# Optimization experiments

Hardware: AMD Instinct MI355X
Metric: run time of the kernel (lower is better)

The kernel has to match this reference:

```python
import jax, jax.numpy as jnp
import numpy as np

B, T = 1024, 39
NUM_C, NUM_STU, NUM_E, EMB = 123, 100000, 50000, 256
H = 123
IN1 = NUM_C + EMB  # 379


def setup_inputs() -> dict:
    key = jax.random.key(0)
    ks = jax.random.split(key, 32)
    f = lambda k, shp, s: jax.random.normal(k, shp, dtype=jnp.float32) * s
    inp = {}
    inp["q_maritx"] = jax.random.uniform(ks[0], (B, T, NUM_C), dtype=jnp.float32)
    inp["q_maritx_next"] = jax.random.uniform(ks[1], (B, T, NUM_C), dtype=jnp.float32)
    inp["concept"] = jax.random.randint(ks[2], (B, T), 0, NUM_C + 1)
    inp["s_id"] = jax.random.randint(ks[3], (B, 1), 0, NUM_STU + 1)
    inp["e_id"] = jax.random.randint(ks[4], (B, T), 0, NUM_E + 1)
    inp["r"] = jax.random.randint(ks[5], (B, T), 0, 2)
    inp["q_next"] = jax.random.randint(ks[6], (B, T), 0, NUM_E + 1)
    inp["concept_next"] = jax.random.randint(ks[7], (B, T), 0, NUM_C + 1)
    # learned parameters
    inp["emb_problem"] = f(ks[8], (NUM_E + 1, EMB), 1.0)
    inp["student_W"] = f(ks[9], (NUM_STU + 1, NUM_C), 1.0)
    inp["k_diff_W"] = f(ks[10], (NUM_E + 1, NUM_C), 1.0)
    inp["e_disc_W"] = f(ks[11], (NUM_E + 1, 1), 1.0)
    inp["answer_W"] = f(ks[12], (2, EMB), 1.0)
    inp["zz_W"] = f(ks[13], (NUM_C, NUM_C), 0.05)
    inp["zz_b"] = jnp.zeros((NUM_C,), jnp.float32)
    inp["d_t"] = f(ks[14], (1,), 1.0)
    inp["d_e"] = f(ks[15], (1,), 1.0)
    inp["W_ih"] = f(ks[16], (H, IN1), 0.05)
    inp["b_ih"] = jnp.zeros((H,), jnp.float32)
    inp["W_hh"] = f(ks[17], (H, H), 0.05)
    inp["b_hh"] = jnp.zeros((H,), jnp.float32)
    inp["W_tg"] = f(ks[18], (H, 1), 0.05)
    inp["b_tg"] = jnp.zeros((H,), jnp.float32)
    inp["W_z"] = f(ks[19], (H, IN1 + H), 0.05)
    inp["b_z"] = jnp.zeros((H,), jnp.float32)
    inp["W_h"] = f(ks[20], (H, IN1 + H), 0.05)
    inp["b_h"] = jnp.zeros((H,), jnp.float32)
    inp["p1_W"] = f(ks[21], (256, 502), 0.05)
    inp["p1_b"] = jnp.zeros((256,), jnp.float32)
    inp["p2_W"] = f(ks[22], (123, 256), 0.05)
    inp["p2_b"] = jnp.zeros((123,), jnp.float32)
    inp["p3_W"] = f(ks[23], (1, 123), 0.05)
    inp["p3_b"] = jnp.zeros((1,), jnp.float32)
    return inp


def _forward(q_maritx, q_maritx_next, emb_problem, student_W, k_diff_W, e_disc_W,
             answer_W, zz_W, zz_b, d_t, d_e, W_ih, b_ih, W_hh, b_hh, W_tg, b_tg,
             W_z, b_z, W_h, b_h, p1_W, p1_b, p2_W, p2_b, p3_W, p3_b,
             s_id, e_id, r, q_next):
    Bc, Tc = e_id.shape
    e_next_emb = emb_problem[q_next]                       # [B,T,256]
    s_prof = jax.nn.sigmoid(student_W[s_id])               # [B,1,123] (broadcasts vs repeat(1,39,1))
    k_diff = jax.nn.sigmoid(k_diff_W[e_id])                # [B,T,123]
    e_disc = jax.nn.sigmoid(e_disc_W[e_id]) * d_e          # [B,T,1]
    r_emb = answer_W[r]                                    # [B,T,256]
    concept_ab = jnp.einsum('btk,hk->bth', q_maritx, zz_W) + zz_b  # [B,T,123]
    x1 = jnp.concatenate([concept_ab * s_prof, r_emb], axis=-1)    # [B,T,379]
    # --- time-gated RNN: h_t = tanh(W_ih x_t + W_hh h + b) * sigmoid(tg(t)) ---
    Xp = jnp.einsum('bti,hi->bth', x1, W_ih) + b_ih
    tvec = jnp.arange(Tc, dtype=Xp.dtype)[:, None]
    gates = jax.nn.sigmoid(tvec * W_tg[:, 0][None, :] + b_tg)      # [T,123]
    h0 = jnp.zeros((Bc, W_hh.shape[0]), Xp.dtype)

    def step1(h, xs):
        xp, g = xs
        h = jnp.tanh(xp + h @ W_hh.T + b_hh) * g
        return h, h

    _, ys1 = jax.lax.scan(step1, h0, (Xp.transpose(1, 0, 2), gates))
    out_zz = ys1.transpose(1, 0, 2)                        # [B,T,123]
    # --- GRU-like cell (W_r unused in original forward) ---
    input_x1 = e_disc * (d_t * s_prof + (1.0 - d_t) * out_zz - k_diff) * q_maritx
    x2 = jnp.concatenate([input_x1, r_emb], axis=-1)       # [B,T,379]
    nin = x2.shape[-1]
    Wz_x, Wz_h = W_z[:, :nin], W_z[:, nin:]
    Wh_x, Wh_h = W_h[:, :nin], W_h[:, nin:]
    Zx = jnp.einsum('bti,hi->bth', x2, Wz_x) + b_z
    Hx = jnp.einsum('bti,hi->bth', x2, Wh_x) + b_h

    def step2(h, xs):
        zx, hx = xs
        z = jax.nn.sigmoid(zx + h @ Wz_h.T)
        ht = jnp.tanh(hx + h @ Wh_h.T)
        h = (1.0 - z) * h + z * ht
        return h, h

    _, ys2 = jax.lax.scan(step2, h0, (Zx.transpose(1, 0, 2), Hx.transpose(1, 0, 2)))
    outputs = ys2.transpose(1, 0, 2)                       # [B,T,123]
    hcat = jnp.concatenate([outputs, e_next_emb, q_maritx_next], axis=-1)  # [B,T,502]
    o1 = jax.nn.sigmoid(hcat @ p1_W.T + p1_b)  # dropout as identity (deterministic reference)
    o2 = jax.nn.sigmoid(o1 @ p2_W.T + p2_b)
    return jax.nn.sigmoid(o2 @ p3_W.T + p3_b)              # [B,T,1]


def reference(q_maritx, q_maritx_next, emb_problem, student_W, k_diff_W, e_disc_W,
              answer_W, zz_W, zz_b, d_t, d_e, W_ih, b_ih, W_hh, b_hh, W_tg, b_tg,
              W_z, b_z, W_h, b_h, p1_W, p1_b, p2_W, p2_b, p3_W, p3_b,
              concept, s_id, e_id, r, q_next, concept_next):
    # concept / concept_next embeddings are computed but unused in the original output
    return _forward(q_maritx, q_maritx_next, emb_problem, student_W, k_diff_W,
                    e_disc_W, answer_W, zz_W, zz_b, d_t, d_e, W_ih, b_ih, W_hh,
                    b_hh, W_tg, b_tg, W_z, b_z, W_h, b_h, p1_W, p1_b, p2_W,
                    p2_b, p3_W, p3_b, s_id, e_id, r, q_next)
```

## Files before the change

kernel.cpp:

```cpp
#include <hip/hip_runtime.h>
#include <hip/hip_bf16.h>

#define NRB 39936
#define BB 1024
#define TT 39
#define CC 123
#define EMBD 256
#define PCH 136

typedef __attribute__((ext_vector_type(8))) short short8;
typedef __attribute__((ext_vector_type(4))) float floatx4;
typedef unsigned short us;

__device__ __forceinline__ float rcp_(float x){ return __builtin_amdgcn_rcpf(x); }
__device__ __forceinline__ float fsig(float x){ return rcp_(1.f + __expf(-x)); }
__device__ __forceinline__ float ftanh(float x){
  float ax = __builtin_fabsf(x);
  float e = __expf(-2.f*ax);
  float r = (1.f - e) * rcp_(1.f + e);
  return __builtin_copysignf(r, x);
}
__device__ __forceinline__ us f2bf(float x){
  union { float f; unsigned u; } v; v.f = x;
  unsigned r = v.u + 0x7FFFu + ((v.u >> 16) & 1u);
  return (us)(r >> 16);
}
__device__ __forceinline__ float bf2f(us u){
  union { unsigned u; float f; } v; v.u = ((unsigned)u) << 16; return v.f;
}

__device__ __forceinline__ void gl_lds16(void* lds, const void* g){
  __builtin_amdgcn_global_load_lds(
      (const __attribute__((address_space(1))) unsigned int*)g,
      (__attribute__((address_space(3))) unsigned int*)lds, 16, 0, 0);
}

#define G_RC 6
#define G_CW 1088
#define G_CAST 2496
#define G_HCAT 1872
#define G_PRE (G_RC + G_CW + G_CAST + G_HCAT)

__global__ __launch_bounds__(256) void k_pre(
    const float* __restrict__ W_ih, const float* __restrict__ W_z,
    const float* __restrict__ W_h, const float* __restrict__ answer_W,
    const float* __restrict__ zz_W, const float* __restrict__ W_hh,
    const float* __restrict__ p1_W, const float* __restrict__ p2_W,
    const float* __restrict__ emb, const int* __restrict__ q_next,
    const float* __restrict__ qmn, const float* __restrict__ q_m,
    float* __restrict__ rtab, us* __restrict__ wts,
    us* __restrict__ p1bf, us* __restrict__ p2bf,
    us* __restrict__ qbf, us* __restrict__ Abf)
{
  const int blk = blockIdx.x, tid = threadIdx.x;
  if (blk < G_RC){
    int which = blk >> 1, j = blk & 1, h = tid;
    if (h >= CC) return;
    const float* W; int stride;
    if (which==0){ W=W_ih; stride=379; } else if (which==1){ W=W_z; stride=502; } else { W=W_h; stride=502; }
    const float* a = answer_W + j*EMBD;
    const float* w = W + (size_t)h*stride + CC;
    float acc = 0.f;
    #pragma unroll 8
    for (int i=0;i<EMBD;i++) acc += w[i]*a[i];
    rtab[(which*2+j)*128 + h] = acc;
    return;
  }
  if (blk < G_RC + G_CW){
    int i = (blk - G_RC)*256 + tid;
    if (i < 7*16384){
      int w = i >> 14, idx = i & 16383, n = idx >> 7, k = idx & 127;
      float v = 0.f;
      if (n < CC && k < CC){
        if      (w==0) v = zz_W[n*CC + k];
        else if (w==1) v = W_ih[n*379 + k];
        else if (w==2) v = W_z [n*502 + k];
        else if (w==3) v = W_h [n*502 + k];
        else if (w==4) v = W_hh[n*CC + k];
        else if (w==5) v = W_z [n*502 + 379 + k];
        else           v = W_h [n*502 + 379 + k];
      }
      wts[i] = f2bf(v);
      return;
    }
    int j = i - 7*16384;
    if (j < 256*512){
      int n = j >> 9, k = j & 511;
      float v;
      if      (k < 379) v = p1_W[n*502 + k + 123];
      else if (k < 384) v = 0.f;
      else if (k < 507) v = p1_W[n*502 + (k - 384)];
      else              v = 0.f;
      p1bf[j] = f2bf(v);
      return;
    }
    j -= 256*512;
    if (j < 128*256){
      int n = j >> 8, k = j & 255;
      p2bf[j] = f2bf(n < CC ? p2_W[n*256 + k] : 0.f);
    }
    return;
  }
  if (blk < G_RC + G_CW + G_CAST){
    const size_t total = (size_t)NRB*128;
    for (size_t i = (size_t)(blk - G_RC - G_CW)*256 + tid; i < total; i += (size_t)G_CAST*256){
      int col = (int)(i & 127); size_t rp = i >> 7;
      int t = (int)(rp >> 10), b = (int)(rp & 1023);
      float v = (col < CC) ? q_m[((size_t)b*TT + t)*CC + col] : 0.f;
      qbf[i] = f2bf(v);
    }
    return;
  }
  {
    const size_t nchunk = (size_t)NRB*48;
    for (size_t c = (size_t)(blk - G_RC - G_CW - G_CAST)*256 + tid; c < nchunk; c += (size_t)G_HCAT*256){
      size_t row = c / 48;
      int c0 = (int)(c - row*48) * 8;
      short8 o;
      if (c0 < 256){
        int qn = q_next[row];
        float4 v0 = *(const float4*)(emb + (size_t)qn*EMBD + c0);
        float4 v1 = *(const float4*)(emb + (size_t)qn*EMBD + c0 + 4);
        o[0]=f2bf(v0.x); o[1]=f2bf(v0.y); o[2]=f2bf(v0.z); o[3]=f2bf(v0.w);
        o[4]=f2bf(v1.x); o[5]=f2bf(v1.y); o[6]=f2bf(v1.z); o[7]=f2bf(v1.w);
      } else {
        int j0 = c0 - 256;
        #pragma unroll
        for (int jj=0;jj<8;jj++){
          int j = j0 + jj;
          o[jj] = (j < CC) ? f2bf(qmn[row*CC + j]) : (short)0;
        }
      }
      *(short8*)(Abf + row*512 + c0) = o;
    }
  }
}

__global__ __launch_bounds__(256) void k_zz_elem(
    const us* __restrict__ X, const us* __restrict__ W,
    const float* __restrict__ zz_b,
    const float* __restrict__ q_m, const int* __restrict__ s_id,
    const int* __restrict__ e_id, const float* __restrict__ student_W,
    const float* __restrict__ k_diff_W, const float* __restrict__ e_disc_W,
    const float* __restrict__ d_t_p, const float* __restrict__ d_e_p,
    us* __restrict__ x1a, us* __restrict__ pre2, us* __restrict__ cqb)
{
  __shared__ __align__(16) us Asl[16][64][8];
  const int tid = threadIdx.x, w = tid >> 6, l = tid & 63, q = l >> 4, r16 = l & 15;
  const int rTile = blockIdx.x*64;
  short8 bfr[2][4];
  #pragma unroll
  for (int nt=0;nt<2;nt++){
    int n = w*32 + nt*16 + r16;
    #pragma unroll
    for (int kt=0;kt<4;kt++)
      bfr[nt][kt] = *(const short8*)(W + (size_t)n*128 + kt*32 + q*8);
  }
  #pragma unroll
  for (int i=0;i<4;i++){
    int seg = i*4 + w;
    gl_lds16(&Asl[seg][l][0], X + (size_t)(rTile+l)*128 + seg*8);
  }
  floatx4 acc[4][2];
  #pragma unroll
  for (int mt=0;mt<4;mt++){
    #pragma unroll
    for (int nt=0;nt<2;nt++){ acc[mt][nt][0]=0.f; acc[mt][nt][1]=0.f; acc[mt][nt][2]=0.f; acc[mt][nt][3]=0.f; }
  }
  __syncthreads();
  #pragma unroll
  for (int kt=0;kt<4;kt++){
    short8 af[4];
    #pragma unroll
    for (int mt=0;mt<4;mt++) af[mt] = *(const short8*)&Asl[kt*4+q][mt*16+r16][0];
    #pragma unroll
    for (int mt=0;mt<4;mt++){
      #pragma unroll
      for (int nt=0;nt<2;nt++)
        acc[mt][nt] = __builtin_amdgcn_mfma_f32_16x16x32_bf16(af[mt], bfr[nt][kt], acc[mt][nt], 0,0,0);
    }
  }
  const float dt = d_t_p[0], de = d_e_p[0];
  float zzb[2]; int colv[2];
  #pragma unroll
  for (int nt=0;nt<2;nt++){
    int col = w*32 + nt*16 + r16; colv[nt] = col;
    zzb[nt] = (col < CC) ? zz_b[col] : 0.f;
  }
  const int t = rTile >> 10;
  #pragma unroll
  for (int mt=0;mt<4;mt++){
    #pragma unroll
    for (int i=0;i<4;i++){
      int row = rTile + mt*16 + q*4 + i;
      int b = row & 1023;
      int g = b*TT + t;
      int btile = b >> 4, r = b & 15;
      int sid = s_id[b];
      int e   = e_id[g];
      float ed = fsig(e_disc_W[e]) * de;
      size_t base = ((size_t)t*64 + btile)*2048;
      #pragma unroll
      for (int nt=0;nt<2;nt++){
        int col = colv[nt];
        float x1v = 0.f, p2v = 0.f, cqv = 0.f;
        if (col < CC){
          float ab = acc[mt][nt][i] + zzb[nt];
          float sp = fsig(student_W[(size_t)sid*CC + col]);
          float kd = fsig(k_diff_W[(size_t)e*CC + col]);
          float qv = q_m[(size_t)g*CC + col];
          x1v = ab*sp;
          p2v = ed*(dt*sp - kd)*qv;
          cqv = ed*(1.f - dt)*qv;
        }
        x1a[base + (size_t)(((col>>5)*64 + ((col>>3)&3)*16 + r)*8) + (col&7)] = f2bf(x1v);
        size_t off = base + (size_t)(((col>>5)*64 + ((r>>2))*16 + (col&15))*8) + ((col>>4)&1)*4 + (r&3);
        pre2[off] = f2bf(p2v);
        cqb[off]  = f2bf(cqv);
      }
    }
  }
}

__global__ __launch_bounds__(256,1) void k_mid(
    const us* __restrict__ x1a, const us* __restrict__ pre2, const us* __restrict__ cqb,
    const us* __restrict__ Wih, const us* __restrict__ Whh,
    const us* __restrict__ Wzx, const us* __restrict__ Whx,
    const us* __restrict__ Wzh, const us* __restrict__ Whh2,
    const float* __restrict__ b_ih, const float* __restrict__ b_z, const float* __restrict__ b_h,
    const float* __restrict__ W_tg, const float* __restrict__ b_tg,
    const float* __restrict__ rtab, const int* __restrict__ r_idx,
    us* __restrict__ Abf)
{
  __shared__ __align__(16) us x1s[2][2048];
  __shared__ __align__(16) us p2s[2][2048];
  __shared__ __align__(16) us cqs[2][2048];
  __shared__ __align__(16) us h1s[2][16*PCH];
  __shared__ __align__(16) us x2s[16*PCH];
  __shared__ __align__(16) us h2r[4][16*PCH];
  __shared__ int rint[640];
  const int tid = threadIdx.x, w = tid >> 6, l = tid & 63, q = l >> 4, r16 = l & 15;
  const int bbase = blockIdx.x*16;

  short8 fih[2][4], fhh[2][4], fzx[2][4], fhx[2][4], fzh[2][4], fh2[2][4];
  float bih[2], bz[2], bh[2], wgv[2], bgv[2];
  float r1v[2][2], r2v[2][2], r3v[2][2];
  int colv[2];
  #pragma unroll
  for (int nt=0;nt<2;nt++){
    int n = w*32 + nt*16 + r16; colv[nt] = n;
    #pragma unroll
    for (int kt=0;kt<4;kt++){
      fih[nt][kt] = *(const short8*)(Wih  + (size_t)n*128 + kt*32 + q*8);
      fhh[nt][kt] = *(const short8*)(Whh  + (size_t)n*128 + kt*32 + q*8);
      fzx[nt][kt] = *(const short8*)(Wzx  + (size_t)n*128 + kt*32 + q*8);
      fhx[nt][kt] = *(const short8*)(Whx  + (size_t)n*128 + kt*32 + q*8);
      fzh[nt][kt] = *(const short8*)(Wzh  + (size_t)n*128 + kt*32 + q*8);
      fh2[nt][kt] = *(const short8*)(Whh2 + (size_t)n*128 + kt*32 + q*8);
    }
    bool v = n < CC;
    bih[nt] = v ? b_ih[n] : 0.f;
    bz [nt] = v ? b_z [n] : 0.f;
    bh [nt] = v ? b_h [n] : 0.f;
    wgv[nt] = v ? W_tg[n] : 0.f;
    bgv[nt] = v ? b_tg[n] : 0.f;
    r1v[0][nt] = v ? rtab[0*128+n] : 0.f;  r1v[1][nt] = v ? rtab[1*128+n] : 0.f;
    r2v[0][nt] = v ? rtab[2*128+n] : 0.f;  r2v[1][nt] = v ? rtab[3*128+n] : 0.f;
    r3v[0][nt] = v ? rtab[4*128+n] : 0.f;  r3v[1][nt] = v ? rtab[5*128+n] : 0.f;
  }
  for (int i = tid; i < TT*16; i += 256){
    int t = i >> 4, row = i & 15;
    rint[i] = r_idx[(size_t)(bbase+row)*TT + t];
  }
  for (int i = tid; i < 16*PCH; i += 256){ h1s[0][i] = 0; h2r[3][i] = 0; }
  {
    size_t base = (size_t)blockIdx.x*2048;
    gl_lds16(&x1s[0][tid*8], x1a  + base + tid*8);
    gl_lds16(&p2s[0][tid*8], pre2 + base + tid*8);
    gl_lds16(&cqs[0][tid*8], cqb  + base + tid*8);
  }
  floatx4 hold[2];
  #pragma unroll
  for (int nt=0;nt<2;nt++){ hold[nt][0]=0.f; hold[nt][1]=0.f; hold[nt][2]=0.f; hold[nt][3]=0.f; }
  __syncthreads();

  for (int t=0; t<TT; t++){
    const int cur = t & 1, nxt = cur ^ 1, rb1 = t & 1, wb1 = rb1 ^ 1;
    if (t < TT-1){
      size_t base = ((size_t)(t+1)*64 + blockIdx.x)*2048;
      gl_lds16(&x1s[nxt][tid*8], x1a  + base + tid*8);
      gl_lds16(&p2s[nxt][tid*8], pre2 + base + tid*8);
      gl_lds16(&cqs[nxt][tid*8], cqb  + base + tid*8);
    }
    short8 a1[4], ah[4], a2p[4];
    #pragma unroll
    for (int kt=0;kt<4;kt++){
      a1[kt]  = *(const short8*)&x1s[cur][(kt*64 + l)*8];
      ah[kt]  = *(const short8*)&h1s[rb1][r16*PCH + kt*32 + q*8];
      a2p[kt] = *(const short8*)&h2r[(t+3)&3][r16*PCH + kt*32 + q*8];
    }
    short8 pc8 = *(const short8*)&p2s[cur][(w*64 + l)*8];
    short8 cc8 = *(const short8*)&cqs[cur][(w*64 + l)*8];
    int rs[4];
    #pragma unroll
    for (int i=0;i<4;i++) rs[i] = rint[t*16 + q*4 + i];
    floatx4 acc1[2], az[2], ahh[2];
    #pragma unroll
    for (int nt=0;nt<2;nt++){
      #pragma unroll
      for (int i=0;i<4;i++){
        acc1[nt][i] = bih[nt] + (rs[i] ? r1v[1][nt] : r1v[0][nt]);
        az  [nt][i] = bz [nt] + (rs[i] ? r2v[1][nt] : r2v[0][nt]);
        ahh [nt][i] = bh [nt] + (rs[i] ? r3v[1][nt] : r3v[0][nt]);
      }
    }
    #pragma unroll
    for (int kt=0;kt<4;kt++){
      #pragma unroll
      for (int nt=0;nt<2;nt++){
        acc1[nt] = __builtin_amdgcn_mfma_f32_16x16x32_bf16(a1[kt],  fih[nt][kt], acc1[nt], 0,0,0);
        acc1[nt] = __builtin_amdgcn_mfma_f32_16x16x32_bf16(ah[kt],  fhh[nt][kt], acc1[nt], 0,0,0);
        az [nt]  = __builtin_amdgcn_mfma_f32_16x16x32_bf16(a2p[kt], fzh[nt][kt], az [nt], 0,0,0);
        ahh[nt]  = __builtin_amdgcn_mfma_f32_16x16x32_bf16(a2p[kt], fh2[nt][kt], ahh[nt], 0,0,0);
      }
    }
    #pragma unroll
    for (int nt=0;nt<2;nt++){
      float g = fsig((float)t*wgv[nt] + bgv[nt]);
      #pragma unroll
      for (int i=0;i<4;i++){
        float h1 = ftanh(acc1[nt][i]) * g;
        h1s[wb1][(q*4+i)*PCH + colv[nt]] = f2bf(h1);
        float pcv = bf2f((us)pc8[nt*4+i]);
        float ccv = bf2f((us)cc8[nt*4+i]);
        x2s[(q*4+i)*PCH + colv[nt]] = f2bf(pcv + ccv*h1);
      }
    }
    __syncthreads();
    short8 ax2[4];
    #pragma unroll
    for (int kt=0;kt<4;kt++) ax2[kt] = *(const short8*)&x2s[r16*PCH + kt*32 + q*8];
    #pragma unroll
    for (int kt=0;kt<4;kt++){
      #pragma unroll
      for (int nt=0;nt<2;nt++){
        az [nt] = __builtin_amdgcn_mfma_f32_16x16x32_bf16(ax2[kt], fzx[nt][kt], az [nt], 0,0,0);
        ahh[nt] = __builtin_amdgcn_mfma_f32_16x16x32_bf16(ax2[kt], fhx[nt][kt], ahh[nt], 0,0,0);
      }
    }
    #pragma unroll
    for (int nt=0;nt<2;nt++){
      #pragma unroll
      for (int i=0;i<4;i++){
        float z  = fsig(az[nt][i]);
        float th = ftanh(ahh[nt][i]);
        float hv = hold[nt][i] + z*(th - hold[nt][i]);
        hold[nt][i] = hv;
        h2r[t&3][(q*4+i)*PCH + colv[nt]] = f2bf(hv);
      }
    }
    __syncthreads();
    if ((t & 3) == 3 || t == TT-1){
      int ns = (t & 3) + 1;
      int r = tid >> 4, c8 = tid & 15;
      for (int s=0; s<ns; s++){
        int td = t - (t & 3) + s;
        short8 vch = *(const short8*)&h2r[s][r*PCH + c8*8];
        *(short8*)(Abf + ((size_t)(bbase + r)*TT + td)*512 + 384 + c8*8) = vch;
      }
      __syncthreads();
    }
  }
}

__global__ __launch_bounds__(256) void k_o1_mfma(
    const us* __restrict__ Abf, const us* __restrict__ p1bf,
    const float* __restrict__ p1_b, us* __restrict__ o1bf)
{
  __shared__ __align__(16) us Asl[8][64][8];
  __shared__ __align__(16) us Bsl[8][256][8];
  const int tid = threadIdx.x;
  const int w = tid >> 6, l = tid & 63;
  const int q = l >> 4, r16 = l & 15;
  const int rTile = blockIdx.x * 64;
  floatx4 acc[4][4];
  #pragma unroll
  for (int a=0;a<4;a++){
    #pragma unroll
    for (int b=0;b<4;b++){ acc[a][b][0]=0.f; acc[a][b][1]=0.f; acc[a][b][2]=0.f; acc[a][b][3]=0.f; }
  }
  for (int c = 0; c < 8; c++){
    const int k0 = c*64;
    #pragma unroll
    for (int i=0;i<2;i++){
      int u = i*256 + tid; int seg = u>>6, m = u&63;
      gl_lds16(&Asl[seg][m][0], Abf + (size_t)(rTile+m)*512 + k0 + seg*8);
    }
    #pragma unroll
    for (int i=0;i<8;i++){
      int u = i*256 + tid; int seg = u>>8, n = u&255;
      gl_lds16(&Bsl[seg][n][0], p1bf + (size_t)n*512 + k0 + seg*8);
    }
    __syncthreads();
    #pragma unroll
    for (int ks=0; ks<2; ks++){
      int seg = ks*4 + q;
      short8 af[4], bfr[4];
      #pragma unroll
      for (int mt=0;mt<4;mt++) af[mt] = *(const short8*)&Asl[seg][mt*16 + r16][0];
      #pragma unroll
      for (int nt=0;nt<4;nt++) bfr[nt] = *(const short8*)&Bsl[seg][w*64 + nt*16 + r16][0];
      #pragma unroll
      for (int mt=0;mt<4;mt++){
        #pragma unroll
        for (int nt=0;nt<4;nt++)
          acc[mt][nt] = __builtin_amdgcn_mfma_f32_16x16x32_bf16(af[mt], bfr[nt], acc[mt][nt], 0,0,0);
      }
    }
    __syncthreads();
  }
  #pragma unroll
  for (int nt=0;nt<4;nt++){
    int col = w*64 + nt*16 + r16;
    float bb = p1_b[col];
    #pragma unroll
    for (int mt=0;mt<4;mt++){
      #pragma unroll
      for (int i=0;i<4;i++){
        int row = rTile + mt*16 + q*4 + i;
        o1bf[(size_t)row*256 + col] = f2bf(fsig(acc[mt][nt][i] + bb));
      }
    }
  }
}

__global__ __launch_bounds__(256) void k_o2_mfma(
    const us* __restrict__ o1bf, const us* __restrict__ p2bf,
    const float* __restrict__ p2_b, const float* __restrict__ p3_W,
    const float* __restrict__ p3_b, float* __restrict__ out)
{
  __shared__ __align__(16) us Asl[8][64][8];
  __shared__ __align__(16) us Bsl[8][128][8];
  __shared__ float red[64][4];
  const int tid = threadIdx.x;
  const int w = tid >> 6, l = tid & 63;
  const int q = l >> 4, r16 = l & 15;
  const int rTile = blockIdx.x * 64;
  floatx4 acc[4][2];
  #pragma unroll
  for (int a=0;a<4;a++){
    #pragma unroll
    for (int b=0;b<2;b++){ acc[a][b][0]=0.f; acc[a][b][1]=0.f; acc[a][b][2]=0.f; acc[a][b][3]=0.f; }
  }
  for (int c = 0; c < 4; c++){
    const int k0 = c*64;
    #pragma unroll
    for (int i=0;i<2;i++){
      int u = i*256 + tid; int seg = u>>6, m = u&63;
      gl_lds16(&Asl[seg][m][0], o1bf + (size_t)(rTile+m)*256 + k0 + seg*8);
    }
    #pragma unroll
    for (int i=0;i<4;i++){
      int u = i*256 + tid; int seg = u>>7, n = u&127;
      gl_lds16(&Bsl[seg][n][0], p2bf + (size_t)n*256 + k0 + seg*8);
    }
    __syncthreads();
    #pragma unroll
    for (int ks=0; ks<2; ks++){
      int seg = ks*4 + q;
      short8 af[4], bfr[2];
      #pragma unroll
      for (int mt=0;mt<4;mt++) af[mt] = *(const short8*)&Asl[seg][mt*16 + r16][0];
      #pragma unroll
      for (int nt=0;nt<2;nt++) bfr[nt] = *(const short8*)&Bsl[seg][w*32 + nt*16 + r16][0];
      #pragma unroll
      for (int mt=0;mt<4;mt++){
        #pragma unroll
        for (int nt=0;nt<2;nt++)
          acc[mt][nt] = __builtin_amdgcn_mfma_f32_16x16x32_bf16(af[mt], bfr[nt], acc[mt][nt], 0,0,0);
      }
    }
    __syncthreads();
  }
  const int n0 = w*32 + r16, n1 = n0 + 16;
  const float pb0 = (n0<CC)? p2_b[n0]:0.f, pb1 = (n1<CC)? p2_b[n1]:0.f;
  const float p30 = (n0<CC)? p3_W[n0]:0.f, p31 = (n1<CC)? p3_W[n1]:0.f;
  #pragma unroll
  for (int mt=0;mt<4;mt++){
    #pragma unroll
    for (int i=0;i<4;i++){
      float s = fsig(acc[mt][0][i]+pb0)*p30 + fsig(acc[mt][1][i]+pb1)*p31;
      s += __shfl_xor(s,1,16); s += __shfl_xor(s,2,16);
      s += __shfl_xor(s,4,16); s += __shfl_xor(s,8,16);
      if (r16==0) red[mt*16 + q*4 + i][w] = s;
    }
  }
  __syncthreads();
  if (tid < 64){
    float o = red[tid][0]+red[tid][1]+red[tid][2]+red[tid][3] + p3_b[0];
    out[rTile + tid] = fsig(o);
  }
}

extern "C" void kernel_launch(void* const* d_in, const int* in_sizes, int n_in,
                              void* d_out, int out_size, void* d_ws, size_t ws_size,
                              hipStream_t stream) {
  const float* q_m       = (const float*)d_in[0];
  const float* q_m_next  = (const float*)d_in[1];
  const int*   s_id      = (const int*)d_in[3];
  const int*   e_id      = (const int*)d_in[4];
  const int*   r_idx     = (const int*)d_in[5];
  const int*   q_next    = (const int*)d_in[6];
  const float* emb_problem = (const float*)d_in[8];
  const float* student_W = (const float*)d_in[9];
  const float* k_diff_W  = (const float*)d_in[10];
  const float* e_disc_W  = (const float*)d_in[11];
  const float* answer_W  = (const float*)d_in[12];
  const float* zz_W      = (const float*)d_in[13];
  const float* zz_b      = (const float*)d_in[14];
  const float* d_t       = (const float*)d_in[15];
  const float* d_e       = (const float*)d_in[16];
  const float* W_ih      = (const float*)d_in[17];
  const float* b_ih      = (const float*)d_in[18];
  const float* W_hh      = (const float*)d_in[19];
  const float* W_tg      = (const float*)d_in[21];
  const float* b_tg      = (const float*)d_in[22];
  const float* W_z       = (const float*)d_in[23];
  const float* b_z       = (const float*)d_in[24];
  const float* W_h       = (const float*)d_in[25];
  const float* b_h       = (const float*)d_in[26];
  const float* p1_W      = (const float*)d_in[27];
  const float* p1_b      = (const float*)d_in[28];
  const float* p2_W      = (const float*)d_in[29];
  const float* p2_b      = (const float*)d_in[30];
  const float* p3_W      = (const float*)d_in[31];
  const float* p3_b      = (const float*)d_in[32];

  float* ws   = (float*)d_ws;
  float* rtab = ws;
  us* qbf  = (us*)(ws + 1024);
  us* x1a  = qbf  + (size_t)NRB*128;
  us* pre2 = x1a  + (size_t)NRB*128;
  us* cqb  = pre2 + (size_t)NRB*128;
  us* Abf  = cqb  + (size_t)NRB*128;
  us* o1bf = Abf  + (size_t)NRB*512;
  us* wts  = o1bf + (size_t)NRB*256;
  us* p1bf = wts  + 7*16384;
  us* p2bf = p1bf + 256*512;

  const us* zzWbf  = wts + 0*16384;
  const us* Wih123 = wts + 1*16384;
  const us* Wz123  = wts + 2*16384;
  const us* Wh123  = wts + 3*16384;
  const us* Whhbf  = wts + 4*16384;
  const us* Wzhbf  = wts + 5*16384;
  const us* Whh2bf = wts + 6*16384;

  hipLaunchKernelGGL(k_pre, dim3(G_PRE), dim3(256), 0, stream,
                     W_ih, W_z, W_h, answer_W, zz_W, W_hh, p1_W, p2_W,
                     emb_problem, q_next, q_m_next, q_m,
                     rtab, wts, p1bf, p2bf, qbf, Abf);
  hipLaunchKernelGGL(k_zz_elem, dim3(NRB/64), dim3(256), 0, stream,
                     qbf, zzWbf, zz_b, q_m, s_id, e_id, student_W, k_diff_W,
                     e_disc_W, d_t, d_e, x1a, pre2, cqb);
  hipLaunchKernelGGL(k_mid, dim3(BB/16), dim3(256), 0, stream,
                     x1a, pre2, cqb, Wih123, Whhbf, Wz123, Wh123, Wzhbf, Whh2bf,
                     b_ih, b_z, b_h, W_tg, b_tg, rtab, r_idx, Abf);
  hipLaunchKernelGGL(k_o1_mfma, dim3(NRB/64), dim3(256), 0, stream,
                     Abf, p1bf, p1_b, o1bf);
  hipLaunchKernelGGL(k_o2_mfma, dim3(NRB/64), dim3(256), 0, stream,
                     o1bf, p2bf, p2_b, p3_W, p3_b, (float*)d_out);
}
```

Baseline: 420.5 us.

## Split recurrent kernel across 8 waves and fuse output MLP layers

The recurrent k_mid kernel now runs 512 threads, with each wave owning 16 output columns instead of 32. The input projection for the next timestep is computed with MFMA ahead of the loop-carried dependency, and its operands are prefetched straight into registers rather than through LDS. The h2 history is written to global one step late from a double buffer, replacing the 4-step batch flush and its extra barrier. The o1 and o2 output kernels are fused so the sigmoid(o1) tile stays in LDS, removing a global round trip and a launch; the cost is higher register and LDS pressure per block.

```diff
diff --git a/kernel.cpp b/kernel.cpp
--- a/kernel.cpp
+++ b/kernel.cpp
@@ -9,6 +9,7 @@
 #define PCH 136
 
 typedef __attribute__((ext_vector_type(8))) short short8;
+typedef __attribute__((ext_vector_type(4))) short shortv4;
 typedef __attribute__((ext_vector_type(4))) float floatx4;
 typedef unsigned short us;
 
@@ -222,7 +223,7 @@
   }
 }
 
-__global__ __launch_bounds__(256,1) void k_mid(
+__global__ __launch_bounds__(512,1) void k_mid(
     const us* __restrict__ x1a, const us* __restrict__ pre2, const us* __restrict__ cqb,
     const us* __restrict__ Wih, const us* __restrict__ Whh,
     const us* __restrict__ Wzx, const us* __restrict__ Whx,
@@ -232,153 +233,147 @@
     const float* __restrict__ rtab, const int* __restrict__ r_idx,
     us* __restrict__ Abf)
 {
-  __shared__ __align__(16) us x1s[2][2048];
-  __shared__ __align__(16) us p2s[2][2048];
-  __shared__ __align__(16) us cqs[2][2048];
   __shared__ __align__(16) us h1s[2][16*PCH];
-  __shared__ __align__(16) us x2s[16*PCH];
-  __shared__ __align__(16) us h2r[4][16*PCH];
-  __shared__ int rint[640];
+  __shared__ __align__(16) us x2s[2][16*PCH];
+  __shared__ __align__(16) us h2s[2][16*PCH];
+  __shared__ int rint[TT*16];
   const int tid = threadIdx.x, w = tid >> 6, l = tid & 63, q = l >> 4, r16 = l & 15;
   const int bbase = blockIdx.x*16;
-
-  short8 fih[2][4], fhh[2][4], fzx[2][4], fhx[2][4], fzh[2][4], fh2[2][4];
-  float bih[2], bz[2], bh[2], wgv[2], bgv[2];
-  float r1v[2][2], r2v[2][2], r3v[2][2];
-  int colv[2];
-  #pragma unroll
-  for (int nt=0;nt<2;nt++){
-    int n = w*32 + nt*16 + r16; colv[nt] = n;
-    #pragma unroll
-    for (int kt=0;kt<4;kt++){
-      fih[nt][kt] = *(const short8*)(Wih  + (size_t)n*128 + kt*32 + q*8);
-      fhh[nt][kt] = *(const short8*)(Whh  + (size_t)n*128 + kt*32 + q*8);
-      fzx[nt][kt] = *(const short8*)(Wzx  + (size_t)n*128 + kt*32 + q*8);
-      fhx[nt][kt] = *(const short8*)(Whx  + (size_t)n*128 + kt*32 + q*8);
-      fzh[nt][kt] = *(const short8*)(Wzh  + (size_t)n*128 + kt*32 + q*8);
-      fh2[nt][kt] = *(const short8*)(Whh2 + (size_t)n*128 + kt*32 + q*8);
-    }
-    bool v = n < CC;
-    bih[nt] = v ? b_ih[n] : 0.f;
-    bz [nt] = v ? b_z [n] : 0.f;
-    bh [nt] = v ? b_h [n] : 0.f;
-    wgv[nt] = v ? W_tg[n] : 0.f;
-    bgv[nt] = v ? b_tg[n] : 0.f;
-    r1v[0][nt] = v ? rtab[0*128+n] : 0.f;  r1v[1][nt] = v ? rtab[1*128+n] : 0.f;
-    r2v[0][nt] = v ? rtab[2*128+n] : 0.f;  r2v[1][nt] = v ? rtab[3*128+n] : 0.f;
-    r3v[0][nt] = v ? rtab[4*128+n] : 0.f;  r3v[1][nt] = v ? rtab[5*128+n] : 0.f;
-  }
-  for (int i = tid; i < TT*16; i += 256){
-    int t = i >> 4, row = i & 15;
-    rint[i] = r_idx[(size_t)(bbase+row)*TT + t];
-  }
-  for (int i = tid; i < 16*PCH; i += 256){ h1s[0][i] = 0; h2r[3][i] = 0; }
+  const int n = w*16 + r16;
+
+  short8 fih[4], fhh[4], fzx[4], fhx[4], fzh[4], fh2w[4];
+  #pragma unroll
+  for (int kt=0;kt<4;kt++){
+    size_t wofs = (size_t)n*128 + kt*32 + q*8;
+    fih[kt]  = *(const short8*)(Wih  + wofs);
+    fhh[kt]  = *(const short8*)(Whh  + wofs);
+    fzx[kt]  = *(const short8*)(Wzx  + wofs);
+    fhx[kt]  = *(const short8*)(Whx  + wofs);
+    fzh[kt]  = *(const short8*)(Wzh  + wofs);
+    fh2w[kt] = *(const short8*)(Whh2 + wofs);
+  }
+  const bool vc = n < CC;
+  const float bih = vc? b_ih[n]:0.f, bzv = vc? b_z[n]:0.f, bhv = vc? b_h[n]:0.f;
+  const float wg = vc? W_tg[n]:0.f, bg = vc? b_tg[n]:0.f;
+  const float r10 = vc? rtab[n]:0.f,     r11 = vc? rtab[128+n]:0.f;
+  const float r20 = vc? rtab[256+n]:0.f, r21 = vc? rtab[384+n]:0.f;
+  const float r30 = vc? rtab[512+n]:0.f, r31 = vc? rtab[640+n]:0.f;
+
+  for (int i = tid; i < TT*16; i += 512)
+    rint[i] = r_idx[(size_t)(bbase + (i & 15))*TT + (i >> 4)];
+  for (int i = tid; i < 16*PCH; i += 512){ h1s[1][i] = 0; h2s[1][i] = 0; }
+
+  short8 x1c[4];
+  shortv4 pc4, cc4;
   {
     size_t base = (size_t)blockIdx.x*2048;
-    gl_lds16(&x1s[0][tid*8], x1a  + base + tid*8);
-    gl_lds16(&p2s[0][tid*8], pre2 + base + tid*8);
-    gl_lds16(&cqs[0][tid*8], cqb  + base + tid*8);
-  }
-  floatx4 hold[2];
-  #pragma unroll
-  for (int nt=0;nt<2;nt++){ hold[nt][0]=0.f; hold[nt][1]=0.f; hold[nt][2]=0.f; hold[nt][3]=0.f; }
+    #pragma unroll
+    for (int kt=0;kt<4;kt++)
+      x1c[kt] = *(const short8*)(x1a + base + (size_t)(kt*64 + q*16 + r16)*8);
+    size_t cofs = base + (size_t)((w>>1)*64 + q*16 + r16)*8 + (size_t)(w&1)*4;
+    pc4 = *(const shortv4*)(pre2 + cofs);
+    cc4 = *(const shortv4*)(cqb + cofs);
+  }
   __syncthreads();
 
+  floatx4 accx;
+  #pragma unroll
+  for (int i=0;i<4;i++){ int rs = rint[q*4 + i]; accx[i] = bih + (rs ? r11 : r10); }
+  #pragma unroll
+  for (int kt=0;kt<4;kt++)
+    accx = __builtin_amdgcn_mfma_f32_16x16x32_bf16(x1c[kt], fih[kt], accx, 0,0,0);
+
+  floatx4 hold; hold[0]=0.f; hold[1]=0.f; hold[2]=0.f; hold[3]=0.f;
+
   for (int t=0; t<TT; t++){
-    const int cur = t & 1, nxt = cur ^ 1, rb1 = t & 1, wb1 = rb1 ^ 1;
+    const int pA = t & 1, pO = pA ^ 1;
+    short8 x1n[4]; shortv4 pcn, ccn;
     if (t < TT-1){
       size_t base = ((size_t)(t+1)*64 + blockIdx.x)*2048;
-      gl_lds16(&x1s[nxt][tid*8], x1a  + base + tid*8);
-      gl_lds16(&p2s[nxt][tid*8], pre2 + base + tid*8);
-      gl_lds16(&cqs[nxt][tid*8], cqb  + base + tid*8);
-    }
-    short8 a1[4], ah[4], a2p[4];
+      #pragma unroll
+      for (int kt=0;kt<4;kt++)
+        x1n[kt] = *(const short8*)(x1a + base + (size_t)(kt*64 + q*16 + r16)*8);
+      size_t cofs = base + (size_t)((w>>1)*64 + q*16 + r16)*8 + (size_t)(w&1)*4;
+      pcn = *(const shortv4*)(pre2 + cofs);
+      ccn = *(const shortv4*)(cqb + cofs);
+    }
+    short8 fr1[4];
+    #pragma unroll
+    for (int kt=0;kt<4;kt++)
+      fr1[kt] = *(const short8*)&h1s[pO][r16*PCH + kt*32 + q*8];
+    floatx4 acc1 = accx;
+    #pragma unroll
+    for (int kt=0;kt<4;kt++)
+      acc1 = __builtin_amdgcn_mfma_f32_16x16x32_bf16(fr1[kt], fhh[kt], acc1, 0,0,0);
+    float g = fsig((float)t*wg + bg);
+    #pragma unroll
+    for (int i=0;i<4;i++){
+      float h1v = ftanh(acc1[i]) * g;
+      h1s[pA][(q*4+i)*PCH + n] = f2bf(h1v);
+      float xv = bf2f((us)pc4[i]) + bf2f((us)cc4[i])*h1v;
+      x2s[pA][(q*4+i)*PCH + n] = f2bf(xv);
+    }
+    __syncthreads();
+    if (t >= 1 && tid < 256){
+      int row = tid >> 4, cs = tid & 15;
+      short8 hv8 = *(const short8*)&h2s[pO][row*PCH + cs*8];
+      *(short8*)(Abf + ((size_t)(bbase + row)*TT + (t-1))*512 + 384 + cs*8) = hv8;
+    }
+    short8 fx[4], fh[4];
     #pragma unroll
     for (int kt=0;kt<4;kt++){
-      a1[kt]  = *(const short8*)&x1s[cur][(kt*64 + l)*8];
-      ah[kt]  = *(const short8*)&h1s[rb1][r16*PCH + kt*32 + q*8];
-      a2p[kt] = *(const short8*)&h2r[(t+3)&3][r16*PCH + kt*32 + q*8];
-    }
-    short8 pc8 = *(const short8*)&p2s[cur][(w*64 + l)*8];
-    short8 cc8 = *(const short8*)&cqs[cur][(w*64 + l)*8];
-    int rs[4];
-    #pragma unroll
-    for (int i=0;i<4;i++) rs[i] = rint[t*16 + q*4 + i];
-    floatx4 acc1[2], az[2], ahh[2];
-    #pragma unroll
-    for (int nt=0;nt<2;nt++){
-      #pragma unroll
-      for (int i=0;i<4;i++){
-        acc1[nt][i] = bih[nt] + (rs[i] ? r1v[1][nt] : r1v[0][nt]);
-        az  [nt][i] = bz [nt] + (rs[i] ? r2v[1][nt] : r2v[0][nt]);
-        ahh [nt][i] = bh [nt] + (rs[i] ? r3v[1][nt] : r3v[0][nt]);
-      }
+      fx[kt] = *(const short8*)&x2s[pA][r16*PCH + kt*32 + q*8];
+      fh[kt] = *(const short8*)&h2s[pO][r16*PCH + kt*32 + q*8];
+    }
+    floatx4 az, ahh;
+    #pragma unroll
+    for (int i=0;i<4;i++){
+      int rs = rint[t*16 + q*4 + i];
+      az[i]  = bzv + (rs ? r21 : r20);
+      ahh[i] = bhv + (rs ? r31 : r30);
     }
     #pragma unroll
     for (int kt=0;kt<4;kt++){
-      #pragma unroll
-      for (int nt=0;nt<2;nt++){
-        acc1[nt] = __builtin_amdgcn_mfma_f32_16x16x32_bf16(a1[kt],  fih[nt][kt], acc1[nt], 0,0,0);
-        acc1[nt] = __builtin_amdgcn_mfma_f32_16x16x32_bf16(ah[kt],  fhh[nt][kt], acc1[nt], 0,0,0);
-        az [nt]  = __builtin_amdgcn_mfma_f32_16x16x32_bf16(a2p[kt], fzh[nt][kt], az [nt], 0,0,0);
-        ahh[nt]  = __builtin_amdgcn_mfma_f32_16x16x32_bf16(a2p[kt], fh2[nt][kt], ahh[nt], 0,0,0);
-      }
-    }
-    #pragma unroll
-    for (int nt=0;nt<2;nt++){
-      float g = fsig((float)t*wgv[nt] + bgv[nt]);
-      #pragma unroll
-      for (int i=0;i<4;i++){
-        float h1 = ftanh(acc1[nt][i]) * g;
-        h1s[wb1][(q*4+i)*PCH + colv[nt]] = f2bf(h1);
-        float pcv = bf2f((us)pc8[nt*4+i]);
-        float ccv = bf2f((us)cc8[nt*4+i]);
-        x2s[(q*4+i)*PCH + colv[nt]] = f2bf(pcv + ccv*h1);
-      }
-    }
-    __syncthreads();
-    short8 ax2[4];
-    #pragma unroll
-    for (int kt=0;kt<4;kt++) ax2[kt] = *(const short8*)&x2s[r16*PCH + kt*32 + q*8];
-    #pragma unroll
-    for (int kt=0;kt<4;kt++){
-      #pragma unroll
-      for (int nt=0;nt<2;nt++){
-        az [nt] = __builtin_amdgcn_mfma_f32_16x16x32_bf16(ax2[kt], fzx[nt][kt], az [nt], 0,0,0);
-        ahh[nt] = __builtin_amdgcn_mfma_f32_16x16x32_bf16(ax2[kt], fhx[nt][kt], ahh[nt], 0,0,0);
-      }
-    }
-    #pragma unroll
-    for (int nt=0;nt<2;nt++){
-      #pragma unroll
-      for (int i=0;i<4;i++){
-        float z  = fsig(az[nt][i]);
-        float th = ftanh(ahh[nt][i]);
-        float hv = hold[nt][i] + z*(th - hold[nt][i]);
-        hold[nt][i] = hv;
-        h2r[t&3][(q*4+i)*PCH + colv[nt]] = f2bf(hv);
-      }
-    }
-    __syncthreads();
-    if ((t & 3) == 3 || t == TT-1){
-      int ns = (t & 3) + 1;
-      int r = tid >> 4, c8 = tid & 15;
-      for (int s=0; s<ns; s++){
-        int td = t - (t & 3) + s;
-        short8 vch = *(const short8*)&h2r[s][r*PCH + c8*8];
-        *(short8*)(Abf + ((size_t)(bbase + r)*TT + td)*512 + 384 + c8*8) = vch;
-      }
-      __syncthreads();
-    }
-  }
-}
-
-__global__ __launch_bounds__(256) void k_o1_mfma(
+      az  = __builtin_amdgcn_mfma_f32_16x16x32_bf16(fx[kt], fzx[kt], az, 0,0,0);
+      az  = __builtin_amdgcn_mfma_f32_16x16x32_bf16(fh[kt], fzh[kt], az, 0,0,0);
+      ahh = __builtin_amdgcn_mfma_f32_16x16x32_bf16(fx[kt], fhx[kt], ahh, 0,0,0);
+      ahh = __builtin_amdgcn_mfma_f32_16x16x32_bf16(fh[kt], fh2w[kt], ahh, 0,0,0);
+    }
+    #pragma unroll
+    for (int i=0;i<4;i++){
+      float z  = fsig(az[i]);
+      float th = ftanh(ahh[i]);
+      hold[i] += z*(th - hold[i]);
+      h2s[pA][(q*4+i)*PCH + n] = f2bf(hold[i]);
+    }
+    if (t < TT-1){
+      #pragma unroll
+      for (int i=0;i<4;i++){ int rs = rint[(t+1)*16 + q*4 + i]; accx[i] = bih + (rs ? r11 : r10); }
+      #pragma unroll
+      for (int kt=0;kt<4;kt++)
+        accx = __builtin_amdgcn_mfma_f32_16x16x32_bf16(x1n[kt], fih[kt], accx, 0,0,0);
+      pc4 = pcn; cc4 = ccn;
+    }
+  }
+  __syncthreads();
+  if (tid < 256){
+    int row = tid >> 4, cs = tid & 15;
+    short8 hv8 = *(const short8*)&h2s[(TT-1)&1][row*PCH + cs*8];
+    *(short8*)(Abf + ((size_t)(bbase + row)*TT + (TT-1))*512 + 384 + cs*8) = hv8;
+  }
+}
+
+__global__ __launch_bounds__(256) void k_out(
     const us* __restrict__ Abf, const us* __restrict__ p1bf,
-    const float* __restrict__ p1_b, us* __restrict__ o1bf)
+    const float* __restrict__ p1_b, const us* __restrict__ p2bf,
+    const float* __restrict__ p2_b, const float* __restrict__ p3_W,
+    const float* __restrict__ p3_b, float* __restrict__ out)
 {
-  __shared__ __align__(16) us Asl[8][64][8];
-  __shared__ __align__(16) us Bsl[8][256][8];
+  __shared__ __align__(16) us smem[20480];
+  __shared__ float red[64][4];
+  us* Asl = smem;
+  us* Bsl = smem + 4096;
+  us* o1s = smem;
   const int tid = threadIdx.x;
   const int w = tid >> 6, l = tid & 63;
   const int q = l >> 4, r16 = l & 15;
@@ -394,12 +389,12 @@
     #pragma unroll
     for (int i=0;i<2;i++){
       int u = i*256 + tid; int seg = u>>6, m = u&63;
-      gl_lds16(&Asl[seg][m][0], Abf + (size_t)(rTile+m)*512 + k0 + seg*8);
+      gl_lds16(&Asl[(seg*64 + m)*8], Abf + (size_t)(rTile+m)*512 + k0 + seg*8);
     }
     #pragma unroll
     for (int i=0;i<8;i++){
-      int u = i*256 + tid; int seg = u>>8, n = u&255;
-      gl_lds16(&Bsl[seg][n][0], p1bf + (size_t)n*512 + k0 + seg*8);
+      int u = i*256 + tid; int seg = u>>8, nn = u&255;
+      gl_lds16(&Bsl[(seg*256 + nn)*8], p1bf + (size_t)nn*512 + k0 + seg*8);
     }
     __syncthreads();
     #pragma unroll
@@ -407,9 +402,9 @@
       int seg = ks*4 + q;
       short8 af[4], bfr[4];
       #pragma unroll
-      for (int mt=0;mt<4;mt++) af[mt] = *(const short8*)&Asl[seg][mt*16 + r16][0];
-      #pragma unroll
-      for (int nt=0;nt<4;nt++) bfr[nt] = *(const short8*)&Bsl[seg][w*64 + nt*16 + r16][0];
+      for (int mt=0;mt<4;mt++) af[mt] = *(const short8*)&Asl[(seg*64 + mt*16 + r16)*8];
+      #pragma unroll
+      for (int nt=0;nt<4;nt++) bfr[nt] = *(const short8*)&Bsl[(seg*256 + w*64 + nt*16 + r16)*8];
       #pragma unroll
       for (int mt=0;mt<4;mt++){
         #pragma unroll
@@ -426,61 +421,36 @@
     #pragma unroll
     for (int mt=0;mt<4;mt++){
       #pragma unroll
-      for (int i=0;i<4;i++){
-        int row = rTile + mt*16 + q*4 + i;
-        o1bf[(size_t)row*256 + col] = f2bf(fsig(acc[mt][nt][i] + bb));
-      }
-    }
-  }
-}
-
-__global__ __launch_bounds__(256) void k_o2_mfma(
-    const us* __restrict__ o1bf, const us* __restrict__ p2bf,
-    const float* __restrict__ p2_b, const float* __restrict__ p3_W,
-    const float* __restrict__ p3_b, float* __restrict__ out)
-{
-  __shared__ __align__(16) us Asl[8][64][8];
-  __shared__ __align__(16) us Bsl[8][128][8];
-  __shared__ float red[64][4];
-  const int tid = threadIdx.x;
-  const int w = tid >> 6, l = tid & 63;
-  const int q = l >> 4, r16 = l & 15;
-  const int rTile = blockIdx.x * 64;
-  floatx4 acc[4][2];
-  #pragma unroll
-  for (int a=0;a<4;a++){
-    #pragma unroll
-    for (int b=0;b<2;b++){ acc[a][b][0]=0.f; acc[a][b][1]=0.f; acc[a][b][2]=0.f; acc[a][b][3]=0.f; }
-  }
-  for (int c = 0; c < 4; c++){
-    const int k0 = c*64;
-    #pragma unroll
-    for (int i=0;i<2;i++){
-      int u = i*256 + tid; int seg = u>>6, m = u&63;
-      gl_lds16(&Asl[seg][m][0], o1bf + (size_t)(rTile+m)*256 + k0 + seg*8);
-    }
-    #pragma unroll
-    for (int i=0;i<4;i++){
-      int u = i*256 + tid; int seg = u>>7, n = u&127;
-      gl_lds16(&Bsl[seg][n][0], p2bf + (size_t)n*256 + k0 + seg*8);
-    }
-    __syncthreads();
-    #pragma unroll
-    for (int ks=0; ks<2; ks++){
-      int seg = ks*4 + q;
-      short8 af[4], bfr[2];
-      #pragma unroll
-      for (int mt=0;mt<4;mt++) af[mt] = *(const short8*)&Asl[seg][mt*16 + r16][0];
-      #pragma unroll
-      for (int nt=0;nt<2;nt++) bfr[nt] = *(const short8*)&Bsl[seg][w*32 + nt*16 + r16][0];
-      #pragma unroll
-      for (int mt=0;mt<4;mt++){
-        #pragma unroll
-        for (int nt=0;nt<2;nt++)
-          acc[mt][nt] = __builtin_amdgcn_mfma_f32_16x16x32_bf16(af[mt], bfr[nt], acc[mt][nt], 0,0,0);
-      }
-    }
-    __syncthreads();
+      for (int i=0;i<4;i++)
+        o1s[(mt*16 + q*4 + i)*264 + col] = f2bf(fsig(acc[mt][nt][i] + bb));
+    }
+  }
+  __syncthreads();
+  short8 bf2[2][8];
+  #pragma unroll
+  for (int nt=0;nt<2;nt++){
+    int n2 = w*32 + nt*16 + r16;
+    #pragma unroll
+    for (int kt=0;kt<8;kt++)
+      bf2[nt][kt] = *(const short8*)(p2bf + (size_t)n2*256 + kt*32 + q*8);
+  }
+  floatx4 ac2[4][2];
+  #pragma unroll
+  for (int mt=0;mt<4;mt++){
+    #pragma unroll
+    for (int nt=0;nt<2;nt++){ ac2[mt][nt][0]=0.f; ac2[mt][nt][1]=0.f; ac2[mt][nt][2]=0.f; ac2[mt][nt][3]=0.f; }
+  }
+  #pragma unroll
+  for (int kt=0;kt<8;kt++){
+    short8 af[4];
+    #pragma unroll
+    for (int mt=0;mt<4;mt++) af[mt] = *(const short8*)&o1s[(mt*16 + r16)*264 + kt*32 + q*8];
+    #pragma unroll
+    for (int mt=0;mt<4;mt++){
+      #pragma unroll
+      for (int nt=0;nt<2;nt++)
+        ac2[mt][nt] = __builtin_amdgcn_mfma_f32_16x16x32_bf16(af[mt], bf2[nt][kt], ac2[mt][nt], 0,0,0);
+    }
   }
   const int n0 = w*32 + r16, n1 = n0 + 16;
   const float pb0 = (n0<CC)? p2_b[n0]:0.f, pb1 = (n1<CC)? p2_b[n1]:0.f;
@@ -489,7 +459,7 @@
   for (int mt=0;mt<4;mt++){
     #pragma unroll
     for (int i=0;i<4;i++){
-      float s = fsig(acc[mt][0][i]+pb0)*p30 + fsig(acc[mt][1][i]+pb1)*p31;
+      float s = fsig(ac2[mt][0][i]+pb0)*p30 + fsig(ac2[mt][1][i]+pb1)*p31;
       s += __shfl_xor(s,1,16); s += __shfl_xor(s,2,16);
       s += __shfl_xor(s,4,16); s += __shfl_xor(s,8,16);
       if (r16==0) red[mt*16 + q*4 + i][w] = s;
@@ -543,8 +513,7 @@
   us* pre2 = x1a  + (size_t)NRB*128;
   us* cqb  = pre2 + (size_t)NRB*128;
   us* Abf  = cqb  + (size_t)NRB*128;
-  us* o1bf = Abf  + (size_t)NRB*512;
-  us* wts  = o1bf + (size_t)NRB*256;
+  us* wts  = Abf  + (size_t)NRB*512;
   us* p1bf = wts  + 7*16384;
   us* p2bf = p1bf + 256*512;
 
@@ -563,11 +532,9 @@
   hipLaunchKernelGGL(k_zz_elem, dim3(NRB/64), dim3(256), 0, stream,
                      qbf, zzWbf, zz_b, q_m, s_id, e_id, student_W, k_diff_W,
                      e_disc_W, d_t, d_e, x1a, pre2, cqb);
-  hipLaunchKernelGGL(k_mid, dim3(BB/16), dim3(256), 0, stream,
+  hipLaunchKernelGGL(k_mid, dim3(BB/16), dim3(512), 0, stream,
                      x1a, pre2, cqb, Wih123, Whhbf, Wz123, Wh123, Wzhbf, Whh2bf,
                      b_ih, b_z, b_h, W_tg, b_tg, rtab, r_idx, Abf);
-  hipLaunchKernelGGL(k_o1_mfma, dim3(NRB/64), dim3(256), 0, stream,
-                     Abf, p1bf, p1_b, o1bf);
-  hipLaunchKernelGGL(k_o2_mfma, dim3(NRB/64), dim3(256), 0, stream,
-                     o1bf, p2bf, p2_b, p3_W, p3_b, (float*)d_out);
-}
+  hipLaunchKernelGGL(k_out, dim3(NRB/64), dim3(256), 0, stream,
+                     Abf, p1bf, p1_b, p2bf, p2_b, p3_W, p3_b, (float*)d_out);
+}
```

New measurement: 380.1 us. 1.11x faster.
